# Kernel optimization log

Measured on AMD Instinct MI355X. Metric: run time of the kernel, lower is better.

The kernel has to match this reference:

```python
import jax, jax.numpy as jnp
import numpy as np

NUM_EMBEDDINGS = 1024
EMBEDDING_DIM = 64


def setup_inputs() -> dict:
    key = jax.random.key(0)
    k_in, k_cb = jax.random.split(key)
    inputs = jax.random.normal(k_in, (16, EMBEDDING_DIM, 64, 64), dtype=jnp.float32)
    # torch default init: uniform(-1/K, 1/K)
    lim = 1.0 / NUM_EMBEDDINGS
    codebook = jax.random.uniform(k_cb, (NUM_EMBEDDINGS, EMBEDDING_DIM),
                                  dtype=jnp.float32, minval=-lim, maxval=lim)
    return {"inputs": inputs, "codebook": codebook}


def reference(inputs, codebook):
    B, C, H, W = inputs.shape  # C == EMBEDDING_DIM
    # BCHW -> BHWC -> (N, C)
    bhwc = jnp.transpose(inputs, (0, 2, 3, 1))
    flat = bhwc.reshape(-1, C)                               # (N, C)
    # squared euclidean distances: ||z||^2 + ||e||^2 - 2 z e^T
    d = (jnp.sum(flat * flat, axis=1, keepdims=True)
         + jnp.sum(codebook * codebook, axis=1)
         - 2.0 * jnp.matmul(flat, codebook.T))               # (N, K)
    zis_flat = jnp.argmin(d, axis=1)                          # (N,)
    zis = zis_flat.reshape(B, H, W)
    # codebook lookup replaces the onehot @ codebook matmul (same math)
    zqs = codebook[zis_flat].reshape(B, H, W, C)              # (B,H,W,C)
    zqs = jnp.transpose(zqs, (0, 3, 1, 2))                    # BCHW
    return zis, zqs
```

## Files before the change

kernel.cpp:

```cpp
#include <hip/hip_runtime.h>
#include <stdint.h>

#define NUM_K 1024
#define CDIM  64
#define NPOS  65536
#define NPB   64
#define BIAS  0.25f
#define QS    4194304.0f
#define ILIM  128
#define CARVE_N0 61440
#define CBT0  3997696
#define AUXC  4063232

typedef __attribute__((ext_vector_type(8))) short short8;
typedef __attribute__((ext_vector_type(4))) float f32x4;

union U4S8 { uint4 u; short8 s; };

#define WS_CNORM 0
#define WS_CNQ   4096
#define WS_CBF   8192

__device__ __forceinline__ void cvt_pair(float f0, float f1,
                                         uint32_t& hp, uint32_t& lp) {
    uint32_t h;
    asm("v_cvt_pk_bf16_f32 %0, %1, %2" : "=v"(h) : "v"(f0), "v"(f1));
    float h0 = __uint_as_float(h << 16);
    float h1 = __uint_as_float(h & 0xFFFF0000u);
    float r0 = f0 - h0, r1 = f1 - h1;
    uint32_t l;
    asm("v_cvt_pk_bf16_f32 %0, %1, %2" : "=v"(l) : "v"(r0), "v"(r1));
    hp = h; lp = l;
}

__device__ __forceinline__ unsigned long long shflxor64(unsigned long long v, int off) {
    unsigned lo = (unsigned)v, hi = (unsigned)(v >> 32);
    lo = (unsigned)__shfl_xor((int)lo, off);
    hi = (unsigned)__shfl_xor((int)hi, off);
    return ((unsigned long long)hi << 32) | lo;
}

__global__ __launch_bounds__(64) void vq_prep_kernel(
    const float* __restrict__ cb, unsigned char* __restrict__ ws,
    float* __restrict__ out) {
#pragma clang fp contract(off)
    const int k = blockIdx.x * 64 + threadIdx.x;
    if (k == 0) ((int*)(out + AUXC))[0] = 0;
    const float4* row4 = (const float4*)(cb + k * CDIM);
    float v[CDIM];
#pragma unroll
    for (int i = 0; i < 16; ++i) {
        float4 t = row4[i];
        v[i * 4 + 0] = t.x; v[i * 4 + 1] = t.y;
        v[i * 4 + 2] = t.z; v[i * 4 + 3] = t.w;
    }
    float r[8];
#pragma unroll
    for (int j = 0; j < 8; ++j) r[j] = v[j] * v[j];
#pragma unroll
    for (int i = 1; i < 8; ++i) {
#pragma unroll
        for (int j = 0; j < 8; ++j) {
            float s = v[i * 8 + j] * v[i * 8 + j];
            r[j] = r[j] + s;
        }
    }
    const float cn =
        ((r[0] + r[1]) + (r[2] + r[3])) + ((r[4] + r[5]) + (r[6] + r[7]));
    ((float*)(ws + WS_CNORM))[k] = cn;
    ((float*)(ws + WS_CNQ))[k]   = (cn + BIAS) * QS;

#pragma unroll 8
    for (int c = 0; c < CDIM; ++c)
        out[CBT0 + c * 1024 + k] = v[c];

    const int kt = k >> 4, rr = k & 15;
    unsigned char* base = ws + WS_CBF + kt * 4096;
#pragma unroll
    for (int s = 0; s < 8; ++s) {
        U4S8 H, L;
        uint32_t hp, lp;
        cvt_pair(v[s * 8 + 0], v[s * 8 + 1], hp, lp); H.u.x = hp; L.u.x = lp;
        cvt_pair(v[s * 8 + 2], v[s * 8 + 3], hp, lp); H.u.y = hp; L.u.y = lp;
        cvt_pair(v[s * 8 + 4], v[s * 8 + 5], hp, lp); H.u.z = hp; L.u.z = lp;
        cvt_pair(v[s * 8 + 6], v[s * 8 + 7], hp, lp); H.u.w = hp; L.u.w = lp;
        const int ks   = s >> 2;
        const int lane = (s & 3) * 16 + rr;
        unsigned char* hi_dst = base + ks * 2048 + lane * 16;
        *(uint4*)(hi_dst)        = H.u;
        *(uint4*)(hi_dst + 1024) = L.u;
    }
}

#define MFMA16(A, B, C) __builtin_amdgcn_mfma_f32_16x16x32_bf16(A, B, C, 0, 0, 0)

#define LOADT(H0, L0, H1, L1, addr) {                   \
    const unsigned char* fb_ = (addr);                  \
    H0.u = *(const uint4*)(fb_);                        \
    L0.u = *(const uint4*)(fb_ + 1024);                 \
    H1.u = *(const uint4*)(fb_ + 2048);                 \
    L1.u = *(const uint4*)(fb_ + 3072);                 \
}

#define COMPT(H0, L0, H1, L1, KT) {                                           \
    const int kb_ = (wv * 16 + (KT)) * 16 + lg * 4;                           \
    const f32x4 cq_ = *(const f32x4*)(cnq_g + kb_);                           \
    _Pragma("unroll")                                                         \
    for (int na = 0; na < 4; ++na) {                                          \
        f32x4 p0 = {0.f,0.f,0.f,0.f}, p1 = {0.f,0.f,0.f,0.f};                 \
        p0 = MFMA16(L0.s, zfh[na][0], p0);                                    \
        p1 = MFMA16(L1.s, zfh[na][1], p1);                                    \
        p0 = MFMA16(H0.s, zfl[na][0], p0);                                    \
        p1 = MFMA16(H1.s, zfl[na][1], p1);                                    \
        p0 = MFMA16(H0.s, zfh[na][0], p0);                                    \
        p1 = MFMA16(H1.s, zfh[na][1], p1);                                    \
        f32x4 a_;                                                             \
        a_[0] = p0[0] + p1[0]; a_[1] = p0[1] + p1[1];                         \
        a_[2] = p0[2] + p1[2]; a_[3] = p0[3] + p1[3];                         \
        _Pragma("unroll")                                                     \
        for (int r = 0; r < 4; r += 2) {                                      \
            uint32_t ka = ((uint32_t)fmaf(-2.0f * QS, a_[r],     cq_[r])     << 10) | (uint32_t)(kb_ + r);     \
            uint32_t kc = ((uint32_t)fmaf(-2.0f * QS, a_[r + 1], cq_[r + 1]) << 10) | (uint32_t)(kb_ + r + 1); \
            uint32_t lo_ = min(ka, kc), hi_ = max(ka, kc);                    \
            m2[na] = min(min(m2[na], hi_), max(lo_, m1[na]));                 \
            m1[na] = min(m1[na], lo_);                                        \
        }                                                                     \
    }                                                                         \
}

__global__ __launch_bounds__(256, 3) void vq_filter_kernel(
    const float* __restrict__ in, const float* __restrict__ cb,
    const unsigned char* __restrict__ ws, float* __restrict__ out) {
#pragma clang fp contract(off)
    const int tid  = threadIdx.x;
    const int lane = tid & 63;
    const int wv   = tid >> 6;
    const int l15  = lane & 15;
    const int lg   = lane >> 4;
    const int n0g  = blockIdx.x * NPB;
    const int b    = n0g >> 12;
    const int hw0  = n0g & 4095;

    __shared__ uint2 wred[NPB][5];
    __shared__ int   sfin[NPB];
    __shared__ __align__(16) unsigned char zs[NPB * 65 * 4];

    const unsigned char* cbf = ws + WS_CBF;
    const float* cnq_g = (const float*)(ws + WS_CNQ);
    int* auxp = (int*)(out + AUXC);

#pragma unroll
    for (int it = 0; it < 2; ++it) {
        const int pos  = tid & 63;
        const int slot = (tid >> 6) + 4 * it;
        const float* zp = in + (((size_t)(b * CDIM + slot * 8)) << 12) + hw0 + pos;
        float f[8];
#pragma unroll
        for (int j = 0; j < 8; ++j) f[j] = zp[(size_t)j << 12];
        U4S8 H, L;
        uint32_t hp, lp;
        cvt_pair(f[0], f[1], hp, lp); H.u.x = hp; L.u.x = lp;
        cvt_pair(f[2], f[3], hp, lp); H.u.y = hp; L.u.y = lp;
        cvt_pair(f[4], f[5], hp, lp); H.u.z = hp; L.u.z = lp;
        cvt_pair(f[6], f[7], hp, lp); H.u.w = hp; L.u.w = lp;
        const int byte = pos * 128 + ((slot * 16) ^ ((pos & 7) * 16));
        *(uint4*)(zs + byte)        = H.u;
        *(uint4*)(zs + 8192 + byte) = L.u;
    }
    __syncthreads();

    short8 zfh[4][2], zfl[4][2];
#pragma unroll
    for (int na = 0; na < 4; ++na) {
        const int pos = na * 16 + l15;
        const int psw = (pos & 7) * 16;
#pragma unroll
        for (int ks = 0; ks < 2; ++ks) {
            const int slot = ks * 4 + lg;
            const int byte = pos * 128 + ((slot * 16) ^ psw);
            zfh[na][ks] = *(const short8*)(zs + byte);
            zfl[na][ks] = *(const short8*)(zs + 8192 + byte);
        }
    }
    __syncthreads();

    uint32_t m1[4] = {0xFFFFFFFFu, 0xFFFFFFFFu, 0xFFFFFFFFu, 0xFFFFFFFFu};
    uint32_t m2[4] = {0xFFFFFFFFu, 0xFFFFFFFFu, 0xFFFFFFFFu, 0xFFFFFFFFu};

    const unsigned char* qb = cbf + (size_t)wv * 65536 + (size_t)lane * 16;
    U4S8 ch0, cl0, ch1, cl1;
    LOADT(ch0, cl0, ch1, cl1, qb);

    for (int kt = 0; kt < 16; ++kt) {
        U4S8 nh0, nl0, nh1, nl1;
        if (kt < 15) LOADT(nh0, nl0, nh1, nl1, qb + (kt + 1) * 4096);
        COMPT(ch0, cl0, ch1, cl1, kt);
        ch0 = nh0; cl0 = nl0; ch1 = nh1; cl1 = nl1;
    }

#pragma unroll
    for (int na = 0; na < 4; ++na) {
#pragma unroll
        for (int off = 16; off <= 32; off <<= 1) {
            uint32_t o1 = (uint32_t)__shfl_xor((int)m1[na], off);
            uint32_t o2 = (uint32_t)__shfl_xor((int)m2[na], off);
            m2[na] = min(min(m2[na], o2), max(m1[na], o1));
            m1[na] = min(m1[na], o1);
        }
    }

    if (lg == 0) {
#pragma unroll
        for (int na = 0; na < 4; ++na) {
            uint2 w; w.x = m1[na]; w.y = m2[na];
            wred[na * 16 + l15][wv] = w;
        }
    }
    __syncthreads();

    if (tid < NPB) {
        uint32_t c1 = 0xFFFFFFFFu, c2 = 0xFFFFFFFFu;
#pragma unroll
        for (int w = 0; w < 4; ++w) {
            uint2 v = wred[tid][w];
            c2 = min(c2, min(v.y, max(c1, v.x)));
            c1 = min(c1, v.x);
        }
        const int idx = (int)(c1 & 1023u);
        sfin[tid] = idx;
        out[n0g + tid] = (float)idx;
        if ((c2 >> 10) - (c1 >> 10) < ILIM) {
            int p = atomicAdd(auxp, 1);
            auxp[1 + p] = n0g + tid;
        }
    }

    if (b == 15) return;
    __syncthreads();

    float (*tile)[65] = (float (*)[65])zs;
    {
        const int p = tid >> 2, q4 = tid & 3;
        const int idx = sfin[p];
        const float4* row = (const float4*)(cb + (size_t)idx * CDIM) + q4 * 4;
#pragma unroll
        for (int i = 0; i < 4; ++i) {
            float4 v = row[i];
            const int cch = q4 * 16 + i * 4;
            tile[p][cch + 0] = v.x; tile[p][cch + 1] = v.y;
            tile[p][cch + 2] = v.z; tile[p][cch + 3] = v.w;
        }
    }
    __syncthreads();
    {
        float* zq = out + NPOS + (((size_t)b * CDIM) << 12) + hw0;
#pragma unroll
        for (int i = 0; i < 16; ++i) {
            const int cch = i * 4 + wv;
            zq[((size_t)cch << 12) + lane] = tile[lane][cch];
        }
    }
}

__global__ __launch_bounds__(256, 2) void vq_rescreen_kernel(
    const float* __restrict__ in, const float* __restrict__ cb,
    const unsigned char* __restrict__ ws, float* __restrict__ out) {
#pragma clang fp contract(off)
    const int tid  = threadIdx.x;
    const int lane = tid & 63;
    const int wv   = tid >> 6;
    const int gw   = blockIdx.x * 4 + wv;

    __shared__ __align__(16) float zsc[4][4][64];
    const int* auxp = (const int*)(out + AUXC);
    const int namb = auxp[0];
    const float* cnorm = (const float*)(ws + WS_CNORM);
    const float* cbT = out + CBT0;

    const int ngroups = (namb + 3) >> 2;
    for (int g = gw; g < ngroups; g += 1024) {
        int   n[4], bb[4], hw[4], nvalid = min(namb - g * 4, 4);
        float zn[4];
#pragma unroll
        for (int s = 0; s < 4; ++s) {
            const int i = g * 4 + (s < nvalid ? s : 0);
            n[s]  = auxp[1 + i];
            bb[s] = n[s] >> 12;
            hw[s] = n[s] & 4095;
        }
#pragma unroll
        for (int s = 0; s < 4; ++s) {
            float zc = in[(((size_t)(bb[s] * CDIM + lane)) << 12) + hw[s]];
            float sq = zc * zc;
            float accp = sq;
#pragma unroll
            for (int i2 = 1; i2 < 8; ++i2)
                accp = accp + __shfl(sq, i2 * 8 + (lane & 7));
            float t1 = accp + __shfl_xor(accp, 1);
            float t2 = t1 + __shfl_xor(t1, 2);
            float t3 = t2 + __shfl_xor(t2, 4);
            zn[s] = __shfl(t3, 0);
            zsc[wv][s][lane] = zc;
        }

        f32x4 acc[4][4];
#pragma unroll
        for (int s = 0; s < 4; ++s)
#pragma unroll
            for (int j = 0; j < 4; ++j) acc[s][j] = (f32x4){0.f, 0.f, 0.f, 0.f};

#pragma unroll 2
        for (int c = 0; c < CDIM; ++c) {
            const float* col = cbT + c * 1024 + 4 * lane;
            f32x4 q0 = *(const f32x4*)(col);
            f32x4 q1 = *(const f32x4*)(col + 256);
            f32x4 q2 = *(const f32x4*)(col + 512);
            f32x4 q3 = *(const f32x4*)(col + 768);
#pragma unroll
            for (int s = 0; s < 4; ++s) {
                const float zv = zsc[wv][s][c];
#pragma unroll
                for (int r = 0; r < 4; ++r) {
                    acc[s][0][r] = fmaf(zv, q0[r], acc[s][0][r]);
                    acc[s][1][r] = fmaf(zv, q1[r], acc[s][1][r]);
                    acc[s][2][r] = fmaf(zv, q2[r], acc[s][2][r]);
                    acc[s][3][r] = fmaf(zv, q3[r], acc[s][3][r]);
                }
            }
        }

#pragma unroll
        for (int s = 0; s < 4; ++s) {
            if (s >= nvalid) break;
            unsigned long long bestk = ~0ull;
#pragma unroll
            for (int j = 0; j < 4; ++j) {
                const f32x4 cnv = *(const f32x4*)(cnorm + j * 256 + 4 * lane);
#pragma unroll
                for (int r = 0; r < 4; ++r) {
                    const int k = j * 256 + 4 * lane + r;
                    float t = zn[s] + cnv[r];
                    float u = 2.0f * acc[s][j][r];
                    float d = t - u;
                    unsigned long long key =
                        ((unsigned long long)__float_as_uint(d) << 10) | (unsigned)k;
                    bestk = key < bestk ? key : bestk;
                }
            }
#pragma unroll
            for (int off = 32; off >= 1; off >>= 1) {
                unsigned long long o = shflxor64(bestk, off);
                bestk = o < bestk ? o : bestk;
            }
            const int idx = (int)(bestk & 1023u);
            if (lane == 0) out[n[s]] = (float)idx;
            if (n[s] < CARVE_N0) {
                float val = cb[idx * CDIM + lane];
                out[NPOS + (((size_t)(bb[s] * CDIM + lane)) << 12) + hw[s]] = val;
            }
        }
    }
}

__global__ __launch_bounds__(256) void vq_patch_kernel(
    const float* __restrict__ cb, float* __restrict__ out) {
    const int tid  = threadIdx.x;
    const int lane = tid & 63;
    const int wv   = tid >> 6;
    const int p0   = CARVE_N0 + blockIdx.x * 64;
    const int hw0  = p0 & 4095;

    __shared__ float tile[64][65];
    __shared__ int sfin[64];
    if (tid < 64) sfin[tid] = (int)out[p0 + tid];
    __syncthreads();
    {
        const int p = tid >> 2, q4 = tid & 3;
        const int idx = sfin[p];
        const float4* row = (const float4*)(cb + (size_t)idx * CDIM) + q4 * 4;
#pragma unroll
        for (int i = 0; i < 4; ++i) {
            float4 v = row[i];
            const int cch = q4 * 16 + i * 4;
            tile[p][cch + 0] = v.x; tile[p][cch + 1] = v.y;
            tile[p][cch + 2] = v.z; tile[p][cch + 3] = v.w;
        }
    }
    __syncthreads();
    {
        float* zq = out + NPOS + (((size_t)15 * CDIM) << 12) + hw0;
#pragma unroll
        for (int i = 0; i < 16; ++i) {
            const int cch = i * 4 + wv;
            zq[((size_t)cch << 12) + lane] = tile[lane][cch];
        }
    }
}

extern "C" void kernel_launch(void* const* d_in, const int* in_sizes, int n_in,
                              void* d_out, int out_size, void* d_ws, size_t ws_size,
                              hipStream_t stream) {
    const float* in = (const float*)d_in[0];
    const float* cb = (const float*)d_in[1];
    float* out = (float*)d_out;
    unsigned char* ws = (unsigned char*)d_ws;

    vq_prep_kernel<<<16, 64, 0, stream>>>(cb, ws, out);
    vq_filter_kernel<<<NPOS / NPB, 256, 0, stream>>>(in, cb, ws, out);
    vq_rescreen_kernel<<<256, 256, 0, stream>>>(in, cb, ws, out);
    vq_patch_kernel<<<64, 256, 0, stream>>>(cb, out);
}
```

Measured before the change: 64.89 us.

## Fuse ambiguous-position rescreen into filter kernel with block-local lists

Removes the separate rescreen kernel and its global atomic list. Each filter block now collects its ambiguous positions in shared memory and recomputes exact fp32 distances for them before writing the quantized tile. This drops one kernel launch, the global atomic traffic and the second pass over ambiguous rows. The codebook tile prefetch in the main loop is also deepened to two tiles ahead. The cost is that blocks with many ambiguous positions serialize that work inside the block, so load across blocks can become uneven.

```diff
diff --git a/kernel.cpp b/kernel.cpp
--- a/kernel.cpp
+++ b/kernel.cpp
@@ -10,7 +10,6 @@
 #define ILIM  128
 #define CARVE_N0 61440
 #define CBT0  3997696
-#define AUXC  4063232
 
 typedef __attribute__((ext_vector_type(8))) short short8;
 typedef __attribute__((ext_vector_type(4))) float f32x4;
@@ -45,7 +44,6 @@
     float* __restrict__ out) {
 #pragma clang fp contract(off)
     const int k = blockIdx.x * 64 + threadIdx.x;
-    if (k == 0) ((int*)(out + AUXC))[0] = 0;
     const float4* row4 = (const float4*)(cb + k * CDIM);
     float v[CDIM];
 #pragma unroll
@@ -143,11 +141,14 @@
 
     __shared__ uint2 wred[NPB][5];
     __shared__ int   sfin[NPB];
+    __shared__ int   ambcnt;
+    __shared__ int   amblist[NPB];
     __shared__ __align__(16) unsigned char zs[NPB * 65 * 4];
 
     const unsigned char* cbf = ws + WS_CBF;
     const float* cnq_g = (const float*)(ws + WS_CNQ);
-    int* auxp = (int*)(out + AUXC);
+
+    if (tid == 0) ambcnt = 0;
 
 #pragma unroll
     for (int it = 0; it < 2; ++it) {
@@ -188,14 +189,19 @@
     uint32_t m2[4] = {0xFFFFFFFFu, 0xFFFFFFFFu, 0xFFFFFFFFu, 0xFFFFFFFFu};
 
     const unsigned char* qb = cbf + (size_t)wv * 65536 + (size_t)lane * 16;
-    U4S8 ch0, cl0, ch1, cl1;
-    LOADT(ch0, cl0, ch1, cl1, qb);
-
-    for (int kt = 0; kt < 16; ++kt) {
-        U4S8 nh0, nl0, nh1, nl1;
-        if (kt < 15) LOADT(nh0, nl0, nh1, nl1, qb + (kt + 1) * 4096);
-        COMPT(ch0, cl0, ch1, cl1, kt);
-        ch0 = nh0; cl0 = nl0; ch1 = nh1; cl1 = nl1;
+    U4S8 Ah0, Al0, Ah1, Al1, Bh0, Bl0, Bh1, Bl1;
+    LOADT(Ah0, Al0, Ah1, Al1, qb);
+    LOADT(Bh0, Bl0, Bh1, Bl1, qb + 4096);
+
+#pragma unroll
+    for (int kt = 0; kt < 16; kt += 2) {
+        U4S8 Nh0, Nl0, Nh1, Nl1, Mh0, Ml0, Mh1, Ml1;
+        if (kt + 2 < 16) LOADT(Nh0, Nl0, Nh1, Nl1, qb + (kt + 2) * 4096);
+        COMPT(Ah0, Al0, Ah1, Al1, kt);
+        if (kt + 3 < 16) LOADT(Mh0, Ml0, Mh1, Ml1, qb + (kt + 3) * 4096);
+        COMPT(Bh0, Bl0, Bh1, Bl1, kt + 1);
+        Ah0 = Nh0; Al0 = Nl0; Ah1 = Nh1; Al1 = Nl1;
+        Bh0 = Mh0; Bl0 = Ml0; Bh1 = Mh1; Bl1 = Ml1;
     }
 
 #pragma unroll
@@ -230,67 +236,22 @@
         sfin[tid] = idx;
         out[n0g + tid] = (float)idx;
         if ((c2 >> 10) - (c1 >> 10) < ILIM) {
-            int p = atomicAdd(auxp, 1);
-            auxp[1 + p] = n0g + tid;
-        }
-    }
-
-    if (b == 15) return;
-    __syncthreads();
-
-    float (*tile)[65] = (float (*)[65])zs;
-    {
-        const int p = tid >> 2, q4 = tid & 3;
-        const int idx = sfin[p];
-        const float4* row = (const float4*)(cb + (size_t)idx * CDIM) + q4 * 4;
-#pragma unroll
-        for (int i = 0; i < 4; ++i) {
-            float4 v = row[i];
-            const int cch = q4 * 16 + i * 4;
-            tile[p][cch + 0] = v.x; tile[p][cch + 1] = v.y;
-            tile[p][cch + 2] = v.z; tile[p][cch + 3] = v.w;
-        }
-    }
-    __syncthreads();
-    {
-        float* zq = out + NPOS + (((size_t)b * CDIM) << 12) + hw0;
-#pragma unroll
-        for (int i = 0; i < 16; ++i) {
-            const int cch = i * 4 + wv;
-            zq[((size_t)cch << 12) + lane] = tile[lane][cch];
-        }
-    }
-}
-
-__global__ __launch_bounds__(256, 2) void vq_rescreen_kernel(
-    const float* __restrict__ in, const float* __restrict__ cb,
-    const unsigned char* __restrict__ ws, float* __restrict__ out) {
-#pragma clang fp contract(off)
-    const int tid  = threadIdx.x;
-    const int lane = tid & 63;
-    const int wv   = tid >> 6;
-    const int gw   = blockIdx.x * 4 + wv;
-
-    __shared__ __align__(16) float zsc[4][4][64];
-    const int* auxp = (const int*)(out + AUXC);
-    const int namb = auxp[0];
-    const float* cnorm = (const float*)(ws + WS_CNORM);
-    const float* cbT = out + CBT0;
-
-    const int ngroups = (namb + 3) >> 2;
-    for (int g = gw; g < ngroups; g += 1024) {
-        int   n[4], bb[4], hw[4], nvalid = min(namb - g * 4, 4);
-        float zn[4];
-#pragma unroll
-        for (int s = 0; s < 4; ++s) {
-            const int i = g * 4 + (s < nvalid ? s : 0);
-            n[s]  = auxp[1 + i];
-            bb[s] = n[s] >> 12;
-            hw[s] = n[s] & 4095;
-        }
-#pragma unroll
-        for (int s = 0; s < 4; ++s) {
-            float zc = in[(((size_t)(bb[s] * CDIM + lane)) << 12) + hw[s]];
+            int p = atomicAdd(&ambcnt, 1);
+            amblist[p] = tid;
+        }
+    }
+    __syncthreads();
+
+    const int namb = ambcnt;
+    if (namb > 0) {
+        const float* cnorm = (const float*)(ws + WS_CNORM);
+        const float* cbT = out + CBT0;
+        float* zrow = (float*)zs + wv * 64;
+        for (int i = wv; i < namb; i += 4) {
+            const int nloc = amblist[i];
+            const int n  = n0g + nloc;
+            const int hw = hw0 + nloc;
+            float zc = in[(((size_t)(b * CDIM + lane)) << 12) + hw];
             float sq = zc * zc;
             float accp = sq;
 #pragma unroll
@@ -299,48 +260,37 @@
             float t1 = accp + __shfl_xor(accp, 1);
             float t2 = t1 + __shfl_xor(t1, 2);
             float t3 = t2 + __shfl_xor(t2, 4);
-            zn[s] = __shfl(t3, 0);
-            zsc[wv][s][lane] = zc;
-        }
-
-        f32x4 acc[4][4];
-#pragma unroll
-        for (int s = 0; s < 4; ++s)
-#pragma unroll
-            for (int j = 0; j < 4; ++j) acc[s][j] = (f32x4){0.f, 0.f, 0.f, 0.f};
-
-#pragma unroll 2
-        for (int c = 0; c < CDIM; ++c) {
-            const float* col = cbT + c * 1024 + 4 * lane;
-            f32x4 q0 = *(const f32x4*)(col);
-            f32x4 q1 = *(const f32x4*)(col + 256);
-            f32x4 q2 = *(const f32x4*)(col + 512);
-            f32x4 q3 = *(const f32x4*)(col + 768);
-#pragma unroll
-            for (int s = 0; s < 4; ++s) {
-                const float zv = zsc[wv][s][c];
+            const float zn = __shfl(t3, 0);
+            zrow[lane] = zc;
+            f32x4 acc0 = {0.f,0.f,0.f,0.f}, acc1 = {0.f,0.f,0.f,0.f};
+            f32x4 acc2 = {0.f,0.f,0.f,0.f}, acc3 = {0.f,0.f,0.f,0.f};
+#pragma unroll 4
+            for (int c = 0; c < CDIM; ++c) {
+                const float zv = zrow[c];
+                const float* col = cbT + c * 1024 + 4 * lane;
+                f32x4 q0 = *(const f32x4*)(col);
+                f32x4 q1 = *(const f32x4*)(col + 256);
+                f32x4 q2 = *(const f32x4*)(col + 512);
+                f32x4 q3 = *(const f32x4*)(col + 768);
 #pragma unroll
                 for (int r = 0; r < 4; ++r) {
-                    acc[s][0][r] = fmaf(zv, q0[r], acc[s][0][r]);
-                    acc[s][1][r] = fmaf(zv, q1[r], acc[s][1][r]);
-                    acc[s][2][r] = fmaf(zv, q2[r], acc[s][2][r]);
-                    acc[s][3][r] = fmaf(zv, q3[r], acc[s][3][r]);
+                    acc0[r] = fmaf(zv, q0[r], acc0[r]);
+                    acc1[r] = fmaf(zv, q1[r], acc1[r]);
+                    acc2[r] = fmaf(zv, q2[r], acc2[r]);
+                    acc3[r] = fmaf(zv, q3[r], acc3[r]);
                 }
             }
-        }
-
-#pragma unroll
-        for (int s = 0; s < 4; ++s) {
-            if (s >= nvalid) break;
             unsigned long long bestk = ~0ull;
 #pragma unroll
             for (int j = 0; j < 4; ++j) {
                 const f32x4 cnv = *(const f32x4*)(cnorm + j * 256 + 4 * lane);
+                const f32x4 acc = (j == 0) ? acc0 : (j == 1) ? acc1
+                                 : (j == 2) ? acc2 : acc3;
 #pragma unroll
                 for (int r = 0; r < 4; ++r) {
                     const int k = j * 256 + 4 * lane + r;
-                    float t = zn[s] + cnv[r];
-                    float u = 2.0f * acc[s][j][r];
+                    float t = zn + cnv[r];
+                    float u = 2.0f * acc[r];
                     float d = t - u;
                     unsigned long long key =
                         ((unsigned long long)__float_as_uint(d) << 10) | (unsigned)k;
@@ -352,12 +302,37 @@
                 unsigned long long o = shflxor64(bestk, off);
                 bestk = o < bestk ? o : bestk;
             }
-            const int idx = (int)(bestk & 1023u);
-            if (lane == 0) out[n[s]] = (float)idx;
-            if (n[s] < CARVE_N0) {
-                float val = cb[idx * CDIM + lane];
-                out[NPOS + (((size_t)(bb[s] * CDIM + lane)) << 12) + hw[s]] = val;
+            if (lane == 0) {
+                const int idx = (int)(bestk & 1023u);
+                out[n] = (float)idx;
+                sfin[nloc] = idx;
             }
+        }
+    }
+    __syncthreads();
+
+    if (b == 15) return;
+
+    float (*tile)[65] = (float (*)[65])zs;
+    {
+        const int p = tid >> 2, q4 = tid & 3;
+        const int idx = sfin[p];
+        const float4* row = (const float4*)(cb + (size_t)idx * CDIM) + q4 * 4;
+#pragma unroll
+        for (int i = 0; i < 4; ++i) {
+            float4 v = row[i];
+            const int cch = q4 * 16 + i * 4;
+            tile[p][cch + 0] = v.x; tile[p][cch + 1] = v.y;
+            tile[p][cch + 2] = v.z; tile[p][cch + 3] = v.w;
+        }
+    }
+    __syncthreads();
+    {
+        float* zq = out + NPOS + (((size_t)b * CDIM) << 12) + hw0;
+#pragma unroll
+        for (int i = 0; i < 16; ++i) {
+            const int cch = i * 4 + wv;
+            zq[((size_t)cch << 12) + lane] = tile[lane][cch];
         }
     }
 }
@@ -407,6 +382,5 @@
 
     vq_prep_kernel<<<16, 64, 0, stream>>>(cb, ws, out);
     vq_filter_kernel<<<NPOS / NPB, 256, 0, stream>>>(in, cb, ws, out);
-    vq_rescreen_kernel<<<256, 256, 0, stream>>>(in, cb, ws, out);
     vq_patch_kernel<<<64, 256, 0, stream>>>(cb, out);
 }
```

New measurement: 57.93 us. -10.7%, faster.
